# Kernel tuning notes

Measured on AMD Instinct MI355X. Metric: run time of the kernel, lower is better.

## Reference

```python
import jax, jax.numpy as jnp
import numpy as np

L, B, T, D, V = 2, 16, 20, 768, 30000


def setup_inputs() -> dict:
    key = jax.random.key(0)
    k1, k2, k3, k4 = jax.random.split(key, 4)
    answer_embed = jax.random.normal(k1, (L, B, T, D), dtype=jnp.float32)
    vocab_embed = 0.1 * jax.random.normal(k2, (V, D), dtype=jnp.float32)
    # classifier_transform modeled as Linear(D, D): y = x @ W.T + b
    W = jax.random.normal(k3, (D, D), dtype=jnp.float32) * (1.0 / np.sqrt(D))
    b = jax.random.normal(k4, (D,), dtype=jnp.float32) * 0.01
    return {"answer_embed": answer_embed, "vocab_embed": vocab_embed, "W": W, "b": b}


def reference(answer_embed, vocab_embed, W, b):
    # vocab_classifiers: [V, D] after the linear transform
    vocab_classifiers = vocab_embed @ W.T + b
    # Original: broadcast multiply [L,B,T,D,1]*[1,1,1,D,V] then sum over D.
    # Mathematically identical contraction over D -> [L, B, T, V]
    return jnp.einsum('lbtd,vd->lbtv', answer_embed, vocab_classifiers)
```

## Files before the change

### kernel.cpp

```cpp
#include <hip/hip_runtime.h>

#define KDIM 768
#define MANS 640
#define VV   30000
#define VPAD 30080

typedef __attribute__((ext_vector_type(4)))  float  f32x4;
typedef __attribute__((ext_vector_type(16))) float  f32x16;
typedef __attribute__((ext_vector_type(8)))  __bf16 bf16x8;

__device__ __forceinline__ unsigned short f2bf(float f) {
    union { float f; unsigned int u; } v; v.f = f;
    unsigned int r = v.u + 0x7fffu + ((v.u >> 16) & 1u);
    return (unsigned short)(r >> 16);
}

__device__ __forceinline__ void load_lds16(const unsigned short* g, unsigned short* l) {
    __builtin_amdgcn_global_load_lds(
        (__attribute__((address_space(1))) void*)(void*)g,
        (__attribute__((address_space(3))) void*)l,
        16, 0, 0);
}

#define PREP_CVT 11250
#define PREP_TRN 11394
#define PREP_TOT 11554

__global__ __launch_bounds__(256) void prep(
    const float* __restrict__ vocab, const float* __restrict__ W,
    const float* __restrict__ A, const float* __restrict__ b,
    unsigned short* __restrict__ vocab_bf, unsigned short* __restrict__ Wt_bf,
    float* __restrict__ cvec)
{
    __shared__ float ts[64][65];
    const int blk = blockIdx.x;
    if (blk < PREP_CVT) {
        long i = (long)blk * 256 + threadIdx.x;
        const f32x4* p = (const f32x4*)vocab + i * 2;
        f32x4 v0 = p[0], v1 = p[1];
        ushort4 o0, o1;
        o0.x = f2bf(v0.x); o0.y = f2bf(v0.y); o0.z = f2bf(v0.z); o0.w = f2bf(v0.w);
        o1.x = f2bf(v1.x); o1.y = f2bf(v1.y); o1.z = f2bf(v1.z); o1.w = f2bf(v1.w);
        ((ushort4*)vocab_bf)[i * 2]     = o0;
        ((ushort4*)vocab_bf)[i * 2 + 1] = o1;
    } else if (blk < PREP_TRN) {
        int tb = blk - PREP_CVT;
        int bx = (tb % 12) * 64, by = (tb / 12) * 64;
        int tx = threadIdx.x & 63, tg = threadIdx.x >> 6;
#pragma unroll
        for (int i = 0; i < 16; ++i) {
            int r = tg * 16 + i;
            ts[r][tx] = W[(long)(by + r) * KDIM + bx + tx];
        }
        __syncthreads();
#pragma unroll
        for (int i = 0; i < 16; ++i) {
            int r = tg * 16 + i;
            Wt_bf[(long)(bx + r) * KDIM + by + tx] = f2bf(ts[tx][r]);
        }
    } else {
        int row  = (blk - PREP_TRN) * 4 + (threadIdx.x >> 6);
        int lane = threadIdx.x & 63;
        const float* ap = A + (long)row * KDIM;
        float s = 0.f;
#pragma unroll
        for (int i = 0; i < KDIM / 64; ++i) s += ap[i * 64 + lane] * b[i * 64 + lane];
#pragma unroll
        for (int off = 32; off; off >>= 1) s += __shfl_down(s, off, 64);
        if (lane == 0) cvec[row] = s;
    }
}

template<int TM, int TN, bool A_F32, bool OUT_BF16>
__global__ __launch_bounds__(256) void gemm32(
    const void* __restrict__ Av, const unsigned short* __restrict__ Bp,
    const float* __restrict__ cvec, void* __restrict__ outv,
    int nValid, long outStride)
{
    constexpr int FM = TM / 64, FN = TN / 64;
    constexpr int SA = TM * 8 / 256, SB = TN * 8 / 256;
    __shared__ unsigned short sA[TM * 64];
    __shared__ unsigned short sB[TN * 64];

    const int t    = threadIdx.x;
    const int lane = t & 63;
    const int w    = t >> 6;
    const int wm   = w >> 1;
    const int wn   = w & 1;
    const int half = lane >> 5;
    const int col  = lane & 31;
    const long m0  = (long)blockIdx.x * TM;
    const long n0  = (long)blockIdx.y * TN;

    f32x16 acc[FM][FN];
#pragma unroll
    for (int i = 0; i < FM; ++i)
#pragma unroll
        for (int j = 0; j < FN; ++j)
            acc[i][j] = (f32x16)(0.f);

    const float*          Af = (const float*)Av;
    const unsigned short* Ab = (const unsigned short*)Av;

    for (int k0 = 0; k0 < KDIM; k0 += 64) {
#pragma unroll
        for (int j = 0; j < SA; ++j) {
            int s   = (j * 4 + w) * 64 + lane;
            int row = s >> 3;
            int c   = (s & 7) ^ (row & 7);
            if (A_F32) {
                const float* g = Af + (m0 + row) * KDIM + k0 + c * 8;
                f32x4 v0 = ((const f32x4*)g)[0], v1 = ((const f32x4*)g)[1];
                ushort4 o0, o1;
                o0.x = f2bf(v0.x); o0.y = f2bf(v0.y); o0.z = f2bf(v0.z); o0.w = f2bf(v0.w);
                o1.x = f2bf(v1.x); o1.y = f2bf(v1.y); o1.z = f2bf(v1.z); o1.w = f2bf(v1.w);
                unsigned short* d = &sA[s * 8];
                ((ushort4*)d)[0] = o0; ((ushort4*)d)[1] = o1;
            } else {
                load_lds16(Ab + (m0 + row) * KDIM + k0 + c * 8,
                           &sA[(j * 4 + w) * 64 * 8]);
            }
        }
#pragma unroll
        for (int j = 0; j < SB; ++j) {
            int s   = (j * 4 + w) * 64 + lane;
            int row = s >> 3;
            int c   = (s & 7) ^ (row & 7);
            load_lds16(Bp + (n0 + row) * KDIM + k0 + c * 8,
                       &sB[(j * 4 + w) * 64 * 8]);
        }
        __syncthreads();

#pragma unroll
        for (int g = 0; g < 4; ++g) {
            const int c = g * 2 + half;
            bf16x8 af[FM], bfr[FN];
#pragma unroll
            for (int fm = 0; fm < FM; ++fm) {
                int row = wm * (TM / 2) + fm * 32 + col;
                af[fm]  = *(const bf16x8*)&sA[(row * 8 + (c ^ (row & 7))) * 8];
            }
#pragma unroll
            for (int fn = 0; fn < FN; ++fn) {
                int row = wn * (TN / 2) + fn * 32 + col;
                bfr[fn] = *(const bf16x8*)&sB[(row * 8 + (c ^ (row & 7))) * 8];
            }
#pragma unroll
            for (int fm = 0; fm < FM; ++fm)
#pragma unroll
                for (int fn = 0; fn < FN; ++fn)
                    acc[fm][fn] = __builtin_amdgcn_mfma_f32_32x32x16_bf16(
                        af[fm], bfr[fn], acc[fm][fn], 0, 0, 0);
        }
        __syncthreads();
    }

#pragma unroll
    for (int fm = 0; fm < FM; ++fm)
#pragma unroll
        for (int fn = 0; fn < FN; ++fn) {
            long n = n0 + wn * (TN / 2) + fn * 32 + col;
#pragma unroll
            for (int rg = 0; rg < 16; ++rg) {
                long m  = m0 + wm * (TM / 2) + fm * 32
                        + (rg & 3) + 8 * (rg >> 2) + 4 * half;
                float v = acc[fm][fn][rg];
                if (OUT_BF16) {
                    ((unsigned short*)outv)[m * outStride + n] = f2bf(v);
                } else {
                    if (n < nValid)
                        ((float*)outv)[m * outStride + n] = v + cvec[m];
                }
            }
        }
}

extern "C" void kernel_launch(void* const* d_in, const int* in_sizes, int n_in,
                              void* d_out, int out_size, void* d_ws, size_t ws_size,
                              hipStream_t stream) {
    const float* answer = (const float*)d_in[0];
    const float* vocab  = (const float*)d_in[1];
    const float* W      = (const float*)d_in[2];
    const float* bvec   = (const float*)d_in[3];

    char* ws = (char*)d_ws;
    unsigned short* vocab_bf = (unsigned short*)ws;
    unsigned short* Wt_bf    = (unsigned short*)(ws + 46080000);
    unsigned short* A2_bf    = (unsigned short*)(ws + 46080000 + 1179648);
    float*          cptr     = (float*)(ws + 46080000 + 1179648 + 983040);

    prep<<<PREP_TOT, 256, 0, stream>>>(vocab, W, answer, bvec,
                                       vocab_bf, Wt_bf, cptr);

    gemm32<64, 128, true, true><<<dim3(MANS / 64, KDIM / 128), 256, 0, stream>>>(
        (const void*)answer, Wt_bf, nullptr, (void*)A2_bf, KDIM, KDIM);

    gemm32<128, 128, false, false><<<dim3(MANS / 128, VPAD / 128), 256, 0, stream>>>(
        (const void*)A2_bf, vocab_bf, cptr, d_out, VV, VV);
}
```

Measured before the change: 232.0 us.

## Fuse vocab fp32-to-bf16 conversion into big GEMM and swizzle block order

Removes the separate pass that converts the 30000x768 vocab matrix to bf16 in workspace. The main GEMM now reads fp32 vocab rows directly, converts them in registers and writes them to LDS. This saves a full write and re-read of about 46 MB. The main GEMM also uses a 1D grid remapped so that groups of 8 N-tiles share M tiles for L2 locality, with padded rows clamped. The trade-off is that each vocab tile is now read as fp32 and converted by all 5 M-blocks, adding redundant conversion work and global traffic.

```diff
diff --git a/kernel.cpp b/kernel.cpp
--- a/kernel.cpp
+++ b/kernel.cpp
@@ -3,7 +3,7 @@
 #define KDIM 768
 #define MANS 640
 #define VV   30000
-#define VPAD 30080
+#define NGRP 235
 
 typedef __attribute__((ext_vector_type(4)))  float  f32x4;
 typedef __attribute__((ext_vector_type(16))) float  f32x16;
@@ -22,30 +22,15 @@
         16, 0, 0);
 }
 
-#define PREP_CVT 11250
-#define PREP_TRN 11394
-#define PREP_TOT 11554
-
-__global__ __launch_bounds__(256) void prep(
-    const float* __restrict__ vocab, const float* __restrict__ W,
-    const float* __restrict__ A, const float* __restrict__ b,
-    unsigned short* __restrict__ vocab_bf, unsigned short* __restrict__ Wt_bf,
+__global__ __launch_bounds__(256) void prep_small(
+    const float* __restrict__ W, const float* __restrict__ A,
+    const float* __restrict__ b, unsigned short* __restrict__ Wt_bf,
     float* __restrict__ cvec)
 {
     __shared__ float ts[64][65];
     const int blk = blockIdx.x;
-    if (blk < PREP_CVT) {
-        long i = (long)blk * 256 + threadIdx.x;
-        const f32x4* p = (const f32x4*)vocab + i * 2;
-        f32x4 v0 = p[0], v1 = p[1];
-        ushort4 o0, o1;
-        o0.x = f2bf(v0.x); o0.y = f2bf(v0.y); o0.z = f2bf(v0.z); o0.w = f2bf(v0.w);
-        o1.x = f2bf(v1.x); o1.y = f2bf(v1.y); o1.z = f2bf(v1.z); o1.w = f2bf(v1.w);
-        ((ushort4*)vocab_bf)[i * 2]     = o0;
-        ((ushort4*)vocab_bf)[i * 2 + 1] = o1;
-    } else if (blk < PREP_TRN) {
-        int tb = blk - PREP_CVT;
-        int bx = (tb % 12) * 64, by = (tb / 12) * 64;
+    if (blk < 144) {
+        int bx = (blk % 12) * 64, by = (blk / 12) * 64;
         int tx = threadIdx.x & 63, tg = threadIdx.x >> 6;
 #pragma unroll
         for (int i = 0; i < 16; ++i) {
@@ -59,7 +44,7 @@
             Wt_bf[(long)(bx + r) * KDIM + by + tx] = f2bf(ts[tx][r]);
         }
     } else {
-        int row  = (blk - PREP_TRN) * 4 + (threadIdx.x >> 6);
+        int row  = (blk - 144) * 4 + (threadIdx.x >> 6);
         int lane = threadIdx.x & 63;
         const float* ap = A + (long)row * KDIM;
         float s = 0.f;
@@ -71,14 +56,11 @@
     }
 }
 
-template<int TM, int TN, bool A_F32, bool OUT_BF16>
-__global__ __launch_bounds__(256) void gemm32(
-    const void* __restrict__ Av, const unsigned short* __restrict__ Bp,
-    const float* __restrict__ cvec, void* __restrict__ outv,
-    int nValid, long outStride)
+__global__ __launch_bounds__(256) void gemm_a2(
+    const float* __restrict__ Af, const unsigned short* __restrict__ Bp,
+    unsigned short* __restrict__ outp)
 {
-    constexpr int FM = TM / 64, FN = TN / 64;
-    constexpr int SA = TM * 8 / 256, SB = TN * 8 / 256;
+    constexpr int TM = 64, TN = 128;
     __shared__ unsigned short sA[TM * 64];
     __shared__ unsigned short sB[TN * 64];
 
@@ -92,37 +74,26 @@
     const long m0  = (long)blockIdx.x * TM;
     const long n0  = (long)blockIdx.y * TN;
 
-    f32x16 acc[FM][FN];
-#pragma unroll
-    for (int i = 0; i < FM; ++i)
-#pragma unroll
-        for (int j = 0; j < FN; ++j)
-            acc[i][j] = (f32x16)(0.f);
-
-    const float*          Af = (const float*)Av;
-    const unsigned short* Ab = (const unsigned short*)Av;
+    f32x16 acc[1][2];
+    acc[0][0] = (f32x16)(0.f);
+    acc[0][1] = (f32x16)(0.f);
 
     for (int k0 = 0; k0 < KDIM; k0 += 64) {
 #pragma unroll
-        for (int j = 0; j < SA; ++j) {
+        for (int j = 0; j < 2; ++j) {
             int s   = (j * 4 + w) * 64 + lane;
             int row = s >> 3;
             int c   = (s & 7) ^ (row & 7);
-            if (A_F32) {
-                const float* g = Af + (m0 + row) * KDIM + k0 + c * 8;
-                f32x4 v0 = ((const f32x4*)g)[0], v1 = ((const f32x4*)g)[1];
-                ushort4 o0, o1;
-                o0.x = f2bf(v0.x); o0.y = f2bf(v0.y); o0.z = f2bf(v0.z); o0.w = f2bf(v0.w);
-                o1.x = f2bf(v1.x); o1.y = f2bf(v1.y); o1.z = f2bf(v1.z); o1.w = f2bf(v1.w);
-                unsigned short* d = &sA[s * 8];
-                ((ushort4*)d)[0] = o0; ((ushort4*)d)[1] = o1;
-            } else {
-                load_lds16(Ab + (m0 + row) * KDIM + k0 + c * 8,
-                           &sA[(j * 4 + w) * 64 * 8]);
-            }
-        }
-#pragma unroll
-        for (int j = 0; j < SB; ++j) {
+            const float* g = Af + (m0 + row) * KDIM + k0 + c * 8;
+            f32x4 v0 = ((const f32x4*)g)[0], v1 = ((const f32x4*)g)[1];
+            ushort4 o0, o1;
+            o0.x = f2bf(v0.x); o0.y = f2bf(v0.y); o0.z = f2bf(v0.z); o0.w = f2bf(v0.w);
+            o1.x = f2bf(v1.x); o1.y = f2bf(v1.y); o1.z = f2bf(v1.z); o1.w = f2bf(v1.w);
+            unsigned short* d = &sA[s * 8];
+            ((ushort4*)d)[0] = o0; ((ushort4*)d)[1] = o1;
+        }
+#pragma unroll
+        for (int j = 0; j < 4; ++j) {
             int s   = (j * 4 + w) * 64 + lane;
             int row = s >> 3;
             int c   = (s & 7) ^ (row & 7);
@@ -133,22 +104,116 @@
 
 #pragma unroll
         for (int g = 0; g < 4; ++g) {
-            const int c = g * 2 + half;
-            bf16x8 af[FM], bfr[FN];
-#pragma unroll
-            for (int fm = 0; fm < FM; ++fm) {
-                int row = wm * (TM / 2) + fm * 32 + col;
-                af[fm]  = *(const bf16x8*)&sA[(row * 8 + (c ^ (row & 7))) * 8];
-            }
-#pragma unroll
-            for (int fn = 0; fn < FN; ++fn) {
-                int row = wn * (TN / 2) + fn * 32 + col;
-                bfr[fn] = *(const bf16x8*)&sB[(row * 8 + (c ^ (row & 7))) * 8];
-            }
-#pragma unroll
-            for (int fm = 0; fm < FM; ++fm)
-#pragma unroll
-                for (int fn = 0; fn < FN; ++fn)
+            const int cg = g * 2 + half;
+            int arow = wm * 32 + col;
+            bf16x8 af = *(const bf16x8*)&sA[(arow * 8 + (cg ^ (arow & 7))) * 8];
+#pragma unroll
+            for (int fn = 0; fn < 2; ++fn) {
+                int brow = wn * 64 + fn * 32 + col;
+                bf16x8 bf = *(const bf16x8*)&sB[(brow * 8 + (cg ^ (brow & 7))) * 8];
+                acc[0][fn] = __builtin_amdgcn_mfma_f32_32x32x16_bf16(
+                    af, bf, acc[0][fn], 0, 0, 0);
+            }
+        }
+        __syncthreads();
+    }
+
+#pragma unroll
+    for (int fn = 0; fn < 2; ++fn) {
+        long n = n0 + wn * 64 + fn * 32 + col;
+#pragma unroll
+        for (int rg = 0; rg < 16; ++rg) {
+            long m = m0 + wm * 32 + (rg & 3) + 8 * (rg >> 2) + 4 * half;
+            outp[m * KDIM + n] = f2bf(acc[0][fn][rg]);
+        }
+    }
+}
+
+__global__ __launch_bounds__(256) void gemm_big(
+    const unsigned short* __restrict__ A, const float* __restrict__ Bf,
+    const float* __restrict__ cvec, float* __restrict__ outp)
+{
+    const int id    = blockIdx.x;
+    const int x     = id & 7;
+    const int q     = id >> 3;
+    const int m_idx = q % 5;
+    const int n_grp = (q / 5) * 8 + x;
+    if (n_grp >= NGRP) return;
+
+    __shared__ unsigned short sA[128 * 64];
+    __shared__ unsigned short sB[128 * 64];
+
+    const int t    = threadIdx.x;
+    const int lane = t & 63;
+    const int w    = t >> 6;
+    const int wm   = w >> 1;
+    const int wn   = w & 1;
+    const int half = lane >> 5;
+    const int col  = lane & 31;
+    const long m0  = (long)m_idx * 128;
+    const long n0  = (long)n_grp * 128;
+
+    f32x16 acc[2][2];
+#pragma unroll
+    for (int i = 0; i < 2; ++i)
+#pragma unroll
+        for (int j = 0; j < 2; ++j) acc[i][j] = (f32x16)(0.f);
+
+    const unsigned short* ga[4];
+    unsigned short*       la[4];
+#pragma unroll
+    for (int j = 0; j < 4; ++j) {
+        int s  = (j * 4 + w) * 64 + lane;
+        int row = s >> 3;
+        int c   = (s & 7) ^ (row & 7);
+        ga[j] = A + (m0 + row) * KDIM + c * 8;
+        la[j] = &sA[(j * 4 + w) * 64 * 8];
+    }
+    const float* gb[4];
+    unsigned short* lb[4];
+#pragma unroll
+    for (int j = 0; j < 4; ++j) {
+        int s   = j * 256 + t;
+        int row = s >> 3;
+        int c   = (s & 7) ^ (row & 7);
+        long grow = n0 + row;
+        if (grow > VV - 1) grow = VV - 1;
+        gb[j] = Bf + grow * KDIM + c * 8;
+        lb[j] = &sB[s * 8];
+    }
+
+    for (int k0 = 0; k0 < KDIM; k0 += 64) {
+#pragma unroll
+        for (int j = 0; j < 4; ++j) load_lds16(ga[j] + k0, la[j]);
+#pragma unroll
+        for (int j = 0; j < 4; ++j) {
+            const float* g = gb[j] + k0;
+            f32x4 v0 = ((const f32x4*)g)[0], v1 = ((const f32x4*)g)[1];
+            ushort4 o0, o1;
+            o0.x = f2bf(v0.x); o0.y = f2bf(v0.y); o0.z = f2bf(v0.z); o0.w = f2bf(v0.w);
+            o1.x = f2bf(v1.x); o1.y = f2bf(v1.y); o1.z = f2bf(v1.z); o1.w = f2bf(v1.w);
+            ((ushort4*)lb[j])[0] = o0; ((ushort4*)lb[j])[1] = o1;
+        }
+        __syncthreads();
+
+#pragma unroll
+        for (int g = 0; g < 4; ++g) {
+            const int cg = g * 2 + half;
+            bf16x8 af[2], bfr[2];
+#pragma unroll
+            for (int fm = 0; fm < 2; ++fm) {
+                int row = wm * 64 + fm * 32 + col;
+                af[fm]  = *(const bf16x8*)&sA[(row * 8 + (cg ^ (row & 7))) * 8];
+            }
+#pragma unroll
+            for (int fn = 0; fn < 2; ++fn) {
+                int row = wn * 64 + fn * 32 + col;
+                bfr[fn] = *(const bf16x8*)&sB[(row * 8 + (cg ^ (row & 7))) * 8];
+            }
+#pragma unroll
+            for (int fm = 0; fm < 2; ++fm)
+#pragma unroll
+                for (int fn = 0; fn < 2; ++fn)
                     acc[fm][fn] = __builtin_amdgcn_mfma_f32_32x32x16_bf16(
                         af[fm], bfr[fn], acc[fm][fn], 0, 0, 0);
         }
@@ -156,20 +221,16 @@
     }
 
 #pragma unroll
-    for (int fm = 0; fm < FM; ++fm)
-#pragma unroll
-        for (int fn = 0; fn < FN; ++fn) {
-            long n = n0 + wn * (TN / 2) + fn * 32 + col;
-#pragma unroll
-            for (int rg = 0; rg < 16; ++rg) {
-                long m  = m0 + wm * (TM / 2) + fm * 32
-                        + (rg & 3) + 8 * (rg >> 2) + 4 * half;
-                float v = acc[fm][fn][rg];
-                if (OUT_BF16) {
-                    ((unsigned short*)outv)[m * outStride + n] = f2bf(v);
-                } else {
-                    if (n < nValid)
-                        ((float*)outv)[m * outStride + n] = v + cvec[m];
+    for (int fm = 0; fm < 2; ++fm)
+#pragma unroll
+        for (int fn = 0; fn < 2; ++fn) {
+            long n = n0 + wn * 64 + fn * 32 + col;
+            if (n < VV) {
+#pragma unroll
+                for (int rg = 0; rg < 16; ++rg) {
+                    long m = m0 + wm * 64 + fm * 32
+                           + (rg & 3) + 8 * (rg >> 2) + 4 * half;
+                    outp[m * (long)VV + n] = acc[fm][fn][rg] + cvec[m];
                 }
             }
         }
@@ -184,17 +245,13 @@
     const float* bvec   = (const float*)d_in[3];
 
     char* ws = (char*)d_ws;
-    unsigned short* vocab_bf = (unsigned short*)ws;
-    unsigned short* Wt_bf    = (unsigned short*)(ws + 46080000);
-    unsigned short* A2_bf    = (unsigned short*)(ws + 46080000 + 1179648);
-    float*          cptr     = (float*)(ws + 46080000 + 1179648 + 983040);
-
-    prep<<<PREP_TOT, 256, 0, stream>>>(vocab, W, answer, bvec,
-                                       vocab_bf, Wt_bf, cptr);
-
-    gemm32<64, 128, true, true><<<dim3(MANS / 64, KDIM / 128), 256, 0, stream>>>(
-        (const void*)answer, Wt_bf, nullptr, (void*)A2_bf, KDIM, KDIM);
-
-    gemm32<128, 128, false, false><<<dim3(MANS / 128, VPAD / 128), 256, 0, stream>>>(
-        (const void*)A2_bf, vocab_bf, cptr, d_out, VV, VV);
-}
+    unsigned short* Wt_bf = (unsigned short*)ws;
+    unsigned short* A2_bf = (unsigned short*)(ws + 1179648);
+    float*          cptr  = (float*)(ws + 1179648 + 983040);
+
+    prep_small<<<304, 256, 0, stream>>>(W, answer, bvec, Wt_bf, cptr);
+
+    gemm_a2<<<dim3(MANS / 64, KDIM / 128), 256, 0, stream>>>(answer, Wt_bf, A2_bf);
+
+    gemm_big<<<1200, 256, 0, stream>>>(A2_bf, vocab, cptr, (float*)d_out);
+}
```

Measured after the change: 231.3 us. Within noise of the previous version (-0.3%).
